# Performance work log

Measured on AMD Instinct MI355X. Metric: run time of the kernel, lower is better.

The kernel has to match this reference:

```python
import jax, jax.numpy as jnp
import numpy as np

NUM_NODES = 2   # number of iResNet blocks
H = 256         # internal_size
L = 4           # num_internal_layers (hidden Linear+ELU layers)
D = 2           # inp_size_linear (2D uv coords)
N = 1048576     # number of points (flattened 1024x1024 STMap grid)


def setup_inputs() -> dict:
    key = jax.random.key(0)
    ks = jax.random.split(key, 7)
    scale = 0.8 / np.sqrt(H)  # mimic lipschitz_correction (spectral norm <= 0.8)
    uv = jax.random.normal(ks[0], (N, D), jnp.float32)
    w_in = jax.random.normal(ks[1], (NUM_NODES, D, H), jnp.float32) * (0.8 / np.sqrt(D))
    b_in = jax.random.normal(ks[2], (NUM_NODES, H), jnp.float32) * 0.01
    w_hid = jax.random.normal(ks[3], (NUM_NODES, L, H, H), jnp.float32) * scale
    b_hid = jax.random.normal(ks[4], (NUM_NODES, L, H), jnp.float32) * 0.01
    w_out = jax.random.normal(ks[5], (NUM_NODES, H, D), jnp.float32) * scale
    b_out = jax.random.normal(ks[6], (NUM_NODES, D), jnp.float32) * 0.01
    return {"uv": uv, "w_in": w_in, "b_in": b_in, "w_hid": w_hid,
            "b_hid": b_hid, "w_out": w_out, "b_out": b_out}


def reference(uv, w_in, b_in, w_hid, b_hid, w_out, b_out):
    # Chain of NUM_NODES invertible ResNet blocks (forward / sensor_to_frustum):
    #   x <- x + MLP(x),  MLP = Lin(D,H)+ELU, L x (Lin(H,H)+ELU), Lin(H,D)
    x = uv  # [N, D]
    for i in range(NUM_NODES):
        h = jax.nn.elu(x @ w_in[i] + b_in[i])          # [N, H]
        for l in range(L):
            h = jax.nn.elu(h @ w_hid[i, l] + b_hid[i, l])
        x = x + (h @ w_out[i] + b_out[i])              # residual add, [N, D]
    return x
```

## Files before the change

### kernel.cpp

```cpp
#include <hip/hip_runtime.h>
#include <stdint.h>

typedef short bf16x8 __attribute__((ext_vector_type(8)));
typedef float f32x16 __attribute__((ext_vector_type(16)));
typedef float f32x4  __attribute__((ext_vector_type(4)));
typedef float f32x2  __attribute__((ext_vector_type(2)));

#define NODES  2
#define LAYERS 4
#define HD     256
#define MTILE  256
#define QBYTES 32768
#define NQ     (NODES*LAYERS*4)

__device__ __forceinline__ unsigned short f2bf(float f) {
  unsigned u = __float_as_uint(f);
  u += 0x7fffu + ((u >> 16) & 1u);
  return (unsigned short)(u >> 16);
}
__device__ __forceinline__ float bf2f(unsigned short s) {
  return __uint_as_float(((unsigned)s) << 16);
}
__device__ __forceinline__ float elu1(float v) {
  return v > 0.0f ? v : (__expf(v) - 1.0f);
}
__device__ __forceinline__ unsigned cvtpk(float lo, float hi) {
  unsigned r;
  asm("v_cvt_pk_bf16_f32 %0, %1, %2" : "=v"(r) : "v"(lo), "v"(hi));
  return r;
}
union U8 { bf16x8 v; unsigned u[4]; };

#define GLOAD_LDS16(gsrc, ldst)                                                        \
  __builtin_amdgcn_global_load_lds(                                                    \
      (const __attribute__((address_space(1))) unsigned int*)(gsrc),                   \
      (__attribute__((address_space(3))) unsigned int*)(ldst), 16, 0, 0)

__global__ __launch_bounds__(256) void convw_kernel(const float* __restrict__ w_hid,
                                                    unsigned short* __restrict__ blob) {
  int e = blockIdx.x * 256 + threadIdx.x;
  int nl = e >> 16;
  int k  = (e >> 8) & 255;
  int n  = e & 255;
  float v = w_hid[(nl * 256 + k) * 256 + n];
  int qq  = k >> 6;
  int kc  = (k >> 4) & 3;
  int k16 = k & 15;
  int g   = (k16 >> 2) & 1;
  int i   = (k16 & 3) | ((k16 >> 3) << 2);
  int nf  = n >> 5, l31 = n & 31;
  unsigned boff = ((unsigned)(nl * 4 + qq) << 15)
                + ((unsigned)kc << 13) + ((unsigned)g << 12)
                + ((unsigned)nf << 9) + ((unsigned)l31 << 4) + ((unsigned)i << 1);
  blob[boff >> 1] = f2bf(v);
}

__global__ __launch_bounds__(256, 1) void nld_kernel(
    const float* __restrict__ uv, const float* __restrict__ w_in,
    const float* __restrict__ b_in, const float* __restrict__ b_hid,
    const float* __restrict__ w_out, const float* __restrict__ b_out,
    const unsigned short* __restrict__ blob, float* __restrict__ out, int nrows) {

  __shared__ __attribute__((aligned(16))) char  w_sm[3 * QBYTES];
  __shared__ __attribute__((aligned(16))) float pb_hid[NODES * LAYERS * HD];
  __shared__ __attribute__((aligned(16))) float pb_in[NODES * HD];

  const int t    = threadIdx.x;
  const int lane = t & 63;
  const int wv   = t >> 6;
  const int l31  = lane & 31;
  const int g    = lane >> 5;
  const long row0 = (long)blockIdx.x * MTILE + wv * 64 + l31;
  const long row1 = row0 + 32;

  auto stage = [&](int iq, unsigned dsto) {
    const char* src = (const char*)blob + (size_t)iq * QBYTES + t * 16;
    char* dst = &w_sm[dsto + t * 16];
#pragma unroll
    for (int r = 0; r < 8; ++r) GLOAD_LDS16(src + r * 4096, dst + r * 4096);
  };

  stage(0, 0);
  stage(1, QBYTES);
  for (int i = t; i < NODES * LAYERS * HD; i += 256) pb_hid[i] = b_hid[i];
  for (int i = t; i < NODES * HD; i += 256) pb_in[i] = b_in[i];

  float x00 = 0.f, x01 = 0.f, x10 = 0.f, x11 = 0.f;
  if (row0 < nrows) { f32x2 u = *(const f32x2*)(uv + row0 * 2); x00 = u[0]; x01 = u[1]; }
  if (row1 < nrows) { f32x2 u = *(const f32x2*)(uv + row1 * 2); x10 = u[0]; x11 = u[1]; }
  __syncthreads();

  bf16x8 hb0[16], hb1[16];
  const unsigned fbase = (unsigned)(g * 4096 + l31 * 16);
  unsigned ro = 0, no = QBYTES, fo = 2 * QBYTES;

  for (int nd = 0; nd < NODES; ++nd) {
    {
      const float* wi0 = w_in + nd * 2 * HD;
      const float* wi1 = wi0 + HD;
      const float* bi  = &pb_in[nd * HD];
#pragma unroll
      for (int c = 0; c < 16; ++c) {
        int kb = 16 * c + 4 * g;
        f32x4 a0 = *(const f32x4*)(wi0 + kb);
        f32x4 a1 = *(const f32x4*)(wi0 + kb + 8);
        f32x4 c0 = *(const f32x4*)(wi1 + kb);
        f32x4 c1 = *(const f32x4*)(wi1 + kb + 8);
        f32x4 e0 = *(const f32x4*)(bi + kb);
        f32x4 e1 = *(const f32x4*)(bi + kb + 8);
        float p0[8], p1[8];
#pragma unroll
        for (int j = 0; j < 4; ++j) {
          p0[j]     = elu1(fmaf(x01, c0[j], fmaf(x00, a0[j], e0[j])));
          p0[4 + j] = elu1(fmaf(x01, c1[j], fmaf(x00, a1[j], e1[j])));
          p1[j]     = elu1(fmaf(x11, c0[j], fmaf(x10, a0[j], e0[j])));
          p1[4 + j] = elu1(fmaf(x11, c1[j], fmaf(x10, a1[j], e1[j])));
        }
        U8 q0, q1;
        q0.u[0] = cvtpk(p0[0], p0[1]); q0.u[1] = cvtpk(p0[2], p0[3]);
        q0.u[2] = cvtpk(p0[4], p0[5]); q0.u[3] = cvtpk(p0[6], p0[7]);
        q1.u[0] = cvtpk(p1[0], p1[1]); q1.u[1] = cvtpk(p1[2], p1[3]);
        q1.u[2] = cvtpk(p1[4], p1[5]); q1.u[3] = cvtpk(p1[6], p1[7]);
        hb0[c] = q0.v;
        hb1[c] = q1.v;
      }
    }

    for (int ly = 0; ly < LAYERS; ++ly) {
      const float* bl = &pb_hid[(nd * LAYERS + ly) * HD];
      f32x16 acc0[8], acc1[8];
#pragma unroll
      for (int nf = 0; nf < 8; ++nf) {
        int nb = 32 * nf + 4 * g;
        f32x4 b0 = *(const f32x4*)(bl + nb);
        f32x4 b1 = *(const f32x4*)(bl + nb + 8);
        f32x4 b2 = *(const f32x4*)(bl + nb + 16);
        f32x4 b3 = *(const f32x4*)(bl + nb + 24);
#pragma unroll
        for (int j = 0; j < 4; ++j) {
          acc0[nf][j]      = b0[j]; acc1[nf][j]      = b0[j];
          acc0[nf][4 + j]  = b1[j]; acc1[nf][4 + j]  = b1[j];
          acc0[nf][8 + j]  = b2[j]; acc1[nf][8 + j]  = b2[j];
          acc0[nf][12 + j] = b3[j]; acc1[nf][12 + j] = b3[j];
        }
      }

      const int iq0 = (nd * LAYERS + ly) * 4;
#pragma unroll
      for (int qq = 0; qq < 4; ++qq) {
        int iq = iq0 + qq;
        if (iq == NQ - 1) asm volatile("s_waitcnt vmcnt(0)" ::: "memory");
        else              asm volatile("s_waitcnt vmcnt(8)" ::: "memory");
        __builtin_amdgcn_s_barrier();
        if (iq + 2 < NQ) stage(iq + 2, fo);
        const char* wb = &w_sm[ro + fbase];
        __builtin_amdgcn_s_setprio(1);
#pragma unroll
        for (int kc = 0; kc < 4; ++kc) {
          bf16x8 wf0 = *(const bf16x8*)(wb + kc * 8192 + 0 * 512);
          bf16x8 wf1 = *(const bf16x8*)(wb + kc * 8192 + 1 * 512);
          bf16x8 wf2 = *(const bf16x8*)(wb + kc * 8192 + 2 * 512);
          bf16x8 wf3 = *(const bf16x8*)(wb + kc * 8192 + 3 * 512);
          bf16x8 wf4 = *(const bf16x8*)(wb + kc * 8192 + 4 * 512);
          bf16x8 wf5 = *(const bf16x8*)(wb + kc * 8192 + 5 * 512);
          bf16x8 wf6 = *(const bf16x8*)(wb + kc * 8192 + 6 * 512);
          bf16x8 wf7 = *(const bf16x8*)(wb + kc * 8192 + 7 * 512);
          bf16x8 h0 = hb0[4 * qq + kc], h1 = hb1[4 * qq + kc];
          acc0[0] = __builtin_amdgcn_mfma_f32_32x32x16_bf16(wf0, h0, acc0[0], 0, 0, 0);
          acc1[0] = __builtin_amdgcn_mfma_f32_32x32x16_bf16(wf0, h1, acc1[0], 0, 0, 0);
          acc0[1] = __builtin_amdgcn_mfma_f32_32x32x16_bf16(wf1, h0, acc0[1], 0, 0, 0);
          acc1[1] = __builtin_amdgcn_mfma_f32_32x32x16_bf16(wf1, h1, acc1[1], 0, 0, 0);
          acc0[2] = __builtin_amdgcn_mfma_f32_32x32x16_bf16(wf2, h0, acc0[2], 0, 0, 0);
          acc1[2] = __builtin_amdgcn_mfma_f32_32x32x16_bf16(wf2, h1, acc1[2], 0, 0, 0);
          acc0[3] = __builtin_amdgcn_mfma_f32_32x32x16_bf16(wf3, h0, acc0[3], 0, 0, 0);
          acc1[3] = __builtin_amdgcn_mfma_f32_32x32x16_bf16(wf3, h1, acc1[3], 0, 0, 0);
          acc0[4] = __builtin_amdgcn_mfma_f32_32x32x16_bf16(wf4, h0, acc0[4], 0, 0, 0);
          acc1[4] = __builtin_amdgcn_mfma_f32_32x32x16_bf16(wf4, h1, acc1[4], 0, 0, 0);
          acc0[5] = __builtin_amdgcn_mfma_f32_32x32x16_bf16(wf5, h0, acc0[5], 0, 0, 0);
          acc1[5] = __builtin_amdgcn_mfma_f32_32x32x16_bf16(wf5, h1, acc1[5], 0, 0, 0);
          acc0[6] = __builtin_amdgcn_mfma_f32_32x32x16_bf16(wf6, h0, acc0[6], 0, 0, 0);
          acc1[6] = __builtin_amdgcn_mfma_f32_32x32x16_bf16(wf6, h1, acc1[6], 0, 0, 0);
          acc0[7] = __builtin_amdgcn_mfma_f32_32x32x16_bf16(wf7, h0, acc0[7], 0, 0, 0);
          acc1[7] = __builtin_amdgcn_mfma_f32_32x32x16_bf16(wf7, h1, acc1[7], 0, 0, 0);
        }
        __builtin_amdgcn_s_setprio(0);
        unsigned tmp = ro; ro = no; no = fo; fo = tmp;
      }

#pragma unroll
      for (int nf = 0; nf < 8; ++nf) {
        float e0[16], e1[16];
#pragma unroll
        for (int j = 0; j < 16; ++j) { e0[j] = elu1(acc0[nf][j]); e1[j] = elu1(acc1[nf][j]); }
        U8 p, q, r, s;
        p.u[0] = cvtpk(e0[0],  e0[1]);  p.u[1] = cvtpk(e0[2],  e0[3]);
        p.u[2] = cvtpk(e0[4],  e0[5]);  p.u[3] = cvtpk(e0[6],  e0[7]);
        q.u[0] = cvtpk(e0[8],  e0[9]);  q.u[1] = cvtpk(e0[10], e0[11]);
        q.u[2] = cvtpk(e0[12], e0[13]); q.u[3] = cvtpk(e0[14], e0[15]);
        r.u[0] = cvtpk(e1[0],  e1[1]);  r.u[1] = cvtpk(e1[2],  e1[3]);
        r.u[2] = cvtpk(e1[4],  e1[5]);  r.u[3] = cvtpk(e1[6],  e1[7]);
        s.u[0] = cvtpk(e1[8],  e1[9]);  s.u[1] = cvtpk(e1[10], e1[11]);
        s.u[2] = cvtpk(e1[12], e1[13]); s.u[3] = cvtpk(e1[14], e1[15]);
        hb0[2 * nf] = p.v; hb0[2 * nf + 1] = q.v;
        hb1[2 * nf] = r.v; hb1[2 * nf + 1] = s.v;
      }
    }

    {
      const float* wo = w_out + nd * HD * 2;
      float s00 = 0.f, s01 = 0.f, s10 = 0.f, s11 = 0.f;
#pragma unroll
      for (int c = 0; c < 16; ++c) {
        int kb = 16 * c + 4 * g;
        f32x4 wA0 = *(const f32x4*)(wo + kb * 2);
        f32x4 wA1 = *(const f32x4*)(wo + kb * 2 + 4);
        f32x4 wB0 = *(const f32x4*)(wo + (kb + 8) * 2);
        f32x4 wB1 = *(const f32x4*)(wo + (kb + 8) * 2 + 4);
        bf16x8 h0 = hb0[c], h1 = hb1[c];
#pragma unroll
        for (int j = 0; j < 2; ++j) {
          float f0 = bf2f((unsigned short)h0[2 * j]),     g0 = bf2f((unsigned short)h1[2 * j]);
          float f1 = bf2f((unsigned short)h0[2 * j + 1]), g1 = bf2f((unsigned short)h1[2 * j + 1]);
          float f2 = bf2f((unsigned short)h0[2 * j + 4]), g2 = bf2f((unsigned short)h1[2 * j + 4]);
          float f3 = bf2f((unsigned short)h0[2 * j + 5]), g3 = bf2f((unsigned short)h1[2 * j + 5]);
          const f32x4& wa = j ? wA1 : wA0;
          const f32x4& wbv = j ? wB1 : wB0;
          s00 = fmaf(f0, wa[0], s00);  s01 = fmaf(f0, wa[1], s01);
          s10 = fmaf(g0, wa[0], s10);  s11 = fmaf(g0, wa[1], s11);
          s00 = fmaf(f1, wa[2], s00);  s01 = fmaf(f1, wa[3], s01);
          s10 = fmaf(g1, wa[2], s10);  s11 = fmaf(g1, wa[3], s11);
          s00 = fmaf(f2, wbv[0], s00); s01 = fmaf(f2, wbv[1], s01);
          s10 = fmaf(g2, wbv[0], s10); s11 = fmaf(g2, wbv[1], s11);
          s00 = fmaf(f3, wbv[2], s00); s01 = fmaf(f3, wbv[3], s01);
          s10 = fmaf(g3, wbv[2], s10); s11 = fmaf(g3, wbv[3], s11);
        }
      }
      s00 += __shfl_xor(s00, 32); s01 += __shfl_xor(s01, 32);
      s10 += __shfl_xor(s10, 32); s11 += __shfl_xor(s11, 32);
      float bo0 = b_out[nd * 2 + 0], bo1 = b_out[nd * 2 + 1];
      x00 += s00 + bo0; x01 += s01 + bo1;
      x10 += s10 + bo0; x11 += s11 + bo1;
    }
  }

  if (g == 0) {
    if (row0 < nrows) { f32x2 r; r[0] = x00; r[1] = x01; *(f32x2*)(out + row0 * 2) = r; }
    if (row1 < nrows) { f32x2 r; r[0] = x10; r[1] = x11; *(f32x2*)(out + row1 * 2) = r; }
  }
}

extern "C" void kernel_launch(void* const* d_in, const int* in_sizes, int n_in,
                              void* d_out, int out_size, void* d_ws, size_t ws_size,
                              hipStream_t stream) {
  const float* uv    = (const float*)d_in[0];
  const float* w_in  = (const float*)d_in[1];
  const float* b_in  = (const float*)d_in[2];
  const float* w_hid = (const float*)d_in[3];
  const float* b_hid = (const float*)d_in[4];
  const float* w_out = (const float*)d_in[5];
  const float* b_out = (const float*)d_in[6];
  unsigned short* blob = (unsigned short*)d_ws;

  int whid_elems = in_sizes[3];
  convw_kernel<<<whid_elems / 256, 256, 0, stream>>>(w_hid, blob);

  int N = in_sizes[0] / 2;
  int grid = (N + MTILE - 1) / MTILE;
  nld_kernel<<<grid, 256, 0, stream>>>(uv, w_in, b_in, b_hid, w_out, b_out,
                                       blob, (float*)d_out, N);
}
```

Baseline: 1.434 ms.

## Load MFMA weight fragments directly from global memory instead of LDS staging

Drops the triple-buffered LDS staging of hidden-layer weights (global_load_lds plus barriers) and instead has each wave load its bf16 weight fragments straight from global memory into registers, double-buffered in halves of each 8KB group. This removes the per-quarter block barriers and the LDS traffic. In exchange every wave separately re-reads the weight blob from L2/L1, so the kernel depends on cache bandwidth and global load latency being hidden behind 8 MFMAs.

Result: faster. 1.266 ms (-11.7%).

```diff
diff --git a/kernel.cpp b/kernel.cpp
--- a/kernel.cpp
+++ b/kernel.cpp
@@ -10,8 +10,8 @@
 #define LAYERS 4
 #define HD     256
 #define MTILE  256
-#define QBYTES 32768
-#define NQ     (NODES*LAYERS*4)
+#define GRPB   8192
+#define NGRP   (NODES*LAYERS*16)
 
 __device__ __forceinline__ unsigned short f2bf(float f) {
   unsigned u = __float_as_uint(f);
@@ -30,11 +30,6 @@
   return r;
 }
 union U8 { bf16x8 v; unsigned u[4]; };
-
-#define GLOAD_LDS16(gsrc, ldst)                                                        \
-  __builtin_amdgcn_global_load_lds(                                                    \
-      (const __attribute__((address_space(1))) unsigned int*)(gsrc),                   \
-      (__attribute__((address_space(3))) unsigned int*)(ldst), 16, 0, 0)
 
 __global__ __launch_bounds__(256) void convw_kernel(const float* __restrict__ w_hid,
                                                     unsigned short* __restrict__ blob) {
@@ -55,13 +50,25 @@
   blob[boff >> 1] = f2bf(v);
 }
 
+struct HG { bf16x8 a, b, c, d; };
+
+__device__ __forceinline__ HG load_hg(const char* __restrict__ p) {
+  HG r;
+  r.a = *(const bf16x8*)(p);
+  r.b = *(const bf16x8*)(p + 512);
+  r.c = *(const bf16x8*)(p + 1024);
+  r.d = *(const bf16x8*)(p + 1536);
+  return r;
+}
+
+#define MM(af, h, accv) accv = __builtin_amdgcn_mfma_f32_32x32x16_bf16(af, h, accv, 0, 0, 0)
+
 __global__ __launch_bounds__(256, 1) void nld_kernel(
     const float* __restrict__ uv, const float* __restrict__ w_in,
     const float* __restrict__ b_in, const float* __restrict__ b_hid,
     const float* __restrict__ w_out, const float* __restrict__ b_out,
     const unsigned short* __restrict__ blob, float* __restrict__ out, int nrows) {
 
-  __shared__ __attribute__((aligned(16))) char  w_sm[3 * QBYTES];
   __shared__ __attribute__((aligned(16))) float pb_hid[NODES * LAYERS * HD];
   __shared__ __attribute__((aligned(16))) float pb_in[NODES * HD];
 
@@ -73,15 +80,6 @@
   const long row0 = (long)blockIdx.x * MTILE + wv * 64 + l31;
   const long row1 = row0 + 32;
 
-  auto stage = [&](int iq, unsigned dsto) {
-    const char* src = (const char*)blob + (size_t)iq * QBYTES + t * 16;
-    char* dst = &w_sm[dsto + t * 16];
-#pragma unroll
-    for (int r = 0; r < 8; ++r) GLOAD_LDS16(src + r * 4096, dst + r * 4096);
-  };
-
-  stage(0, 0);
-  stage(1, QBYTES);
   for (int i = t; i < NODES * LAYERS * HD; i += 256) pb_hid[i] = b_hid[i];
   for (int i = t; i < NODES * HD; i += 256) pb_in[i] = b_in[i];
 
@@ -91,8 +89,11 @@
   __syncthreads();
 
   bf16x8 hb0[16], hb1[16];
-  const unsigned fbase = (unsigned)(g * 4096 + l31 * 16);
-  unsigned ro = 0, no = QBYTES, fo = 2 * QBYTES;
+  const unsigned voff = (unsigned)(g * 4096 + l31 * 16);
+  const char* gp   = (const char*)blob;
+  const char* gend = (const char*)blob + (size_t)(NGRP - 1) * GRPB;
+
+  HG A = load_hg(gp + voff);
 
   for (int nd = 0; nd < NODES; ++nd) {
     {
@@ -145,46 +146,22 @@
         }
       }
 
-      const int iq0 = (nd * LAYERS + ly) * 4;
-#pragma unroll
-      for (int qq = 0; qq < 4; ++qq) {
-        int iq = iq0 + qq;
-        if (iq == NQ - 1) asm volatile("s_waitcnt vmcnt(0)" ::: "memory");
-        else              asm volatile("s_waitcnt vmcnt(8)" ::: "memory");
-        __builtin_amdgcn_s_barrier();
-        if (iq + 2 < NQ) stage(iq + 2, fo);
-        const char* wb = &w_sm[ro + fbase];
-        __builtin_amdgcn_s_setprio(1);
-#pragma unroll
-        for (int kc = 0; kc < 4; ++kc) {
-          bf16x8 wf0 = *(const bf16x8*)(wb + kc * 8192 + 0 * 512);
-          bf16x8 wf1 = *(const bf16x8*)(wb + kc * 8192 + 1 * 512);
-          bf16x8 wf2 = *(const bf16x8*)(wb + kc * 8192 + 2 * 512);
-          bf16x8 wf3 = *(const bf16x8*)(wb + kc * 8192 + 3 * 512);
-          bf16x8 wf4 = *(const bf16x8*)(wb + kc * 8192 + 4 * 512);
-          bf16x8 wf5 = *(const bf16x8*)(wb + kc * 8192 + 5 * 512);
-          bf16x8 wf6 = *(const bf16x8*)(wb + kc * 8192 + 6 * 512);
-          bf16x8 wf7 = *(const bf16x8*)(wb + kc * 8192 + 7 * 512);
-          bf16x8 h0 = hb0[4 * qq + kc], h1 = hb1[4 * qq + kc];
-          acc0[0] = __builtin_amdgcn_mfma_f32_32x32x16_bf16(wf0, h0, acc0[0], 0, 0, 0);
-          acc1[0] = __builtin_amdgcn_mfma_f32_32x32x16_bf16(wf0, h1, acc1[0], 0, 0, 0);
-          acc0[1] = __builtin_amdgcn_mfma_f32_32x32x16_bf16(wf1, h0, acc0[1], 0, 0, 0);
-          acc1[1] = __builtin_amdgcn_mfma_f32_32x32x16_bf16(wf1, h1, acc1[1], 0, 0, 0);
-          acc0[2] = __builtin_amdgcn_mfma_f32_32x32x16_bf16(wf2, h0, acc0[2], 0, 0, 0);
-          acc1[2] = __builtin_amdgcn_mfma_f32_32x32x16_bf16(wf2, h1, acc1[2], 0, 0, 0);
-          acc0[3] = __builtin_amdgcn_mfma_f32_32x32x16_bf16(wf3, h0, acc0[3], 0, 0, 0);
-          acc1[3] = __builtin_amdgcn_mfma_f32_32x32x16_bf16(wf3, h1, acc1[3], 0, 0, 0);
-          acc0[4] = __builtin_amdgcn_mfma_f32_32x32x16_bf16(wf4, h0, acc0[4], 0, 0, 0);
-          acc1[4] = __builtin_amdgcn_mfma_f32_32x32x16_bf16(wf4, h1, acc1[4], 0, 0, 0);
-          acc0[5] = __builtin_amdgcn_mfma_f32_32x32x16_bf16(wf5, h0, acc0[5], 0, 0, 0);
-          acc1[5] = __builtin_amdgcn_mfma_f32_32x32x16_bf16(wf5, h1, acc1[5], 0, 0, 0);
-          acc0[6] = __builtin_amdgcn_mfma_f32_32x32x16_bf16(wf6, h0, acc0[6], 0, 0, 0);
-          acc1[6] = __builtin_amdgcn_mfma_f32_32x32x16_bf16(wf6, h1, acc1[6], 0, 0, 0);
-          acc0[7] = __builtin_amdgcn_mfma_f32_32x32x16_bf16(wf7, h0, acc0[7], 0, 0, 0);
-          acc1[7] = __builtin_amdgcn_mfma_f32_32x32x16_bf16(wf7, h1, acc1[7], 0, 0, 0);
-        }
-        __builtin_amdgcn_s_setprio(0);
-        unsigned tmp = ro; ro = no; no = fo; fo = tmp;
+#pragma unroll
+      for (int u = 0; u < 16; ++u) {
+        HG B = load_hg(gp + voff + 2048);
+        bf16x8 h0 = hb0[u], h1 = hb1[u];
+        MM(A.a, h0, acc0[0]); MM(A.a, h1, acc1[0]);
+        MM(A.b, h0, acc0[1]); MM(A.b, h1, acc1[1]);
+        MM(A.c, h0, acc0[2]); MM(A.c, h1, acc1[2]);
+        MM(A.d, h0, acc0[3]); MM(A.d, h1, acc1[3]);
+        const char* nx = gp + GRPB;
+        if (nx > gend) nx = gend;
+        A = load_hg(nx + voff);
+        MM(B.a, h0, acc0[4]); MM(B.a, h1, acc1[4]);
+        MM(B.b, h0, acc0[5]); MM(B.b, h1, acc1[5]);
+        MM(B.c, h0, acc0[6]); MM(B.c, h1, acc1[6]);
+        MM(B.d, h0, acc0[7]); MM(B.d, h1, acc1[7]);
+        gp = nx;
       }
 
 #pragma unroll
```
